# Kernel optimization log

Hardware: AMD Instinct MI355X
Metric: run time of the kernel (lower is better)

## Reference

```python
import jax, jax.numpy as jnp
import numpy as np

NUM_EXPERTS = 64
TOP_K = 2
TEMPERATURE = 1.0
MOMENTUM = 0.9


def _l2norm(x, axis=-1):
    # torch F.normalize: x / max(||x||, eps)
    n = jnp.linalg.norm(x, axis=axis, keepdims=True)
    return x / jnp.maximum(n, 1e-12)


def setup_inputs() -> dict:
    key = jax.random.key(0)
    k1, k2 = jax.random.split(key)
    hidden_states = jax.random.normal(k1, (4, 4096, 2048), dtype=jnp.float32)
    centers = _l2norm(jax.random.normal(k2, (NUM_EXPERTS, 2048), dtype=jnp.float32))
    return {"hidden_states": hidden_states, "centers": centers}


def reference(hidden_states, centers):
    B, T, H = hidden_states.shape
    flat = hidden_states.reshape(-1, H).astype(jnp.float32)  # [N, H]
    N = flat.shape[0]

    # cosine-similarity logits
    reps_n = _l2norm(flat)
    centers_n = _l2norm(centers)
    temp = jnp.maximum(jnp.float32(TEMPERATURE), 1e-6)
    logits = (reps_n @ centers_n.T) / temp  # [N, E]

    probs = jax.nn.softmax(logits, axis=-1)
    top_w, top_ids = jax.lax.top_k(probs, TOP_K)  # [N, k]
    top_w = top_w / (jnp.sum(top_w, axis=-1, keepdims=True) + 1e-9)

    # EMA center update from top-1 routed expert (training+update path)
    route = top_ids[:, 0]  # [N]
    sums = jax.ops.segment_sum(flat, route, num_segments=NUM_EXPERTS)  # [E, H]
    counts = jax.ops.segment_sum(jnp.ones((N, 1), jnp.float32), route,
                                 num_segments=NUM_EXPERTS)  # [E, 1]
    means = sums / (counts + 1e-6)
    updated = _l2norm(MOMENTUM * centers + (1.0 - MOMENTUM) * means)
    new_centers = jnp.where(counts > 0, updated, centers)

    top_ids = top_ids.reshape(B, T, TOP_K)
    top_w = top_w.reshape(B, T, TOP_K)
    return top_ids, top_w, new_centers
```

## Files before the change

kernel.cpp:

```cpp
#include <hip/hip_runtime.h>
#include <math.h>

#define NTOK 16384
#define HDIM 2048
#define NEXP 64
#define KK   32
#define TAU  5e-5f
#define LGT  16384
#define MAXB 2048


__global__ __launch_bounds__(256)
void zero_kernel(float* p, int n) {
  int i = blockIdx.x * 256 + threadIdx.x;
  if (i < n) p[i] = 0.0f;
}

__device__ __forceinline__ float block_reduce_sum(float v, float* red) {
  #pragma unroll
  for (int o = 32; o > 0; o >>= 1) v += __shfl_down(v, o, 64);
  int lane = threadIdx.x & 63;
  int wid  = threadIdx.x >> 6;
  if (lane == 0) red[wid] = v;
  __syncthreads();
  float s = red[0] + red[1] + red[2] + red[3];
  __syncthreads();
  return s;
}

__device__ __forceinline__ double block_reduce_sum_f64(double v, double* red) {
  const int tid = threadIdx.x;
  red[tid] = v;
  __syncthreads();
  if (tid < 128) red[tid] += red[tid + 128];
  __syncthreads();
  if (tid < 64)  red[tid] += red[tid + 64];
  __syncthreads();
  double s = 0.0;
  if (tid < 64) {
    s = red[tid];
    #pragma unroll
    for (int o = 32; o > 0; o >>= 1) s += __shfl_down(s, o, 64);
  }
  if (tid == 0) red[0] = s;
  __syncthreads();
  s = red[0];
  __syncthreads();
  return s;
}

__global__ __launch_bounds__(256)
void cnorm_kernel(const float* __restrict__ c, float* __restrict__ inv_nc) {
  __shared__ float red[4];
  int e = blockIdx.x;
  float ss = 0.f;
  #pragma unroll
  for (int j = 0; j < 8; ++j) {
    float v = c[e * HDIM + threadIdx.x + j * 256];
    ss += v * v;
  }
  float tot = block_reduce_sum(ss, red);
  if (threadIdx.x == 0) inv_nc[e] = 1.0f / fmaxf(sqrtf(tot), 1e-12f);
}

__global__ __launch_bounds__(256)
void cnormalize_kernel(const float* __restrict__ c, float* __restrict__ bn) {
  __shared__ double redd[256];
  __shared__ float s_nc;
  const int e = blockIdx.x;
  const int tid = threadIdx.x;
  const float* cr = c + (size_t)e * HDIM;
  double acc = 0.0;
  #pragma unroll
  for (int i = 0; i < 8; ++i) {
    double v = (double)cr[tid + 256 * i];
    acc += v * v;
  }
  double cn = block_reduce_sum_f64(acc, redd);
  if (tid == 0) s_nc = (float)fmax(sqrt(cn), 1e-12);
  __syncthreads();
  const double nc = (double)s_nc;
  #pragma unroll
  for (int i = 0; i < 8; ++i) {
    int k = tid + 256 * i;
    bn[(size_t)e * HDIM + k] = (float)((double)cr[k] / nc);
  }
}

__global__ __launch_bounds__(256)
void gemm_kernel(const float* __restrict__ x, const float* __restrict__ c,
                 float* __restrict__ logits, float* __restrict__ xnorm2) {
  __shared__ __align__(16) float xs[KK][132];
  __shared__ __align__(16) float cs[KK][68];

  const int tid = threadIdx.x;
  const int mt  = blockIdx.x >> 2;
  const int ks  = blockIdx.x & 3;
  const int t0  = mt * 128;
  const int kb  = ks * 512;
  const int tx  = tid & 15;
  const int ty  = tid >> 4;
  const int r0  = ty * 8;
  const int e0t = tx * 4;
  const int sr = tid >> 1;
  const int sq = (tid & 1) * 16;
  const int er = tid >> 2;
  const int eq = (tid & 3) * 8;

  const float* xrow = x + (size_t)(t0 + sr) * HDIM + kb + sq;
  const float* crow = c + (size_t)er * HDIM + kb + eq;

  float4 xp[4], cp[2];
  #pragma unroll
  for (int i = 0; i < 4; ++i) xp[i] = *(const float4*)(xrow + 4 * i);
  #pragma unroll
  for (int i = 0; i < 2; ++i) cp[i] = *(const float4*)(crow + 4 * i);

  float acc[4][8];
  #pragma unroll
  for (int j = 0; j < 4; ++j)
    #pragma unroll
    for (int i = 0; i < 8; ++i) acc[j][i] = 0.f;
  float nacc = 0.f;

  for (int it = 0; it < 16; ++it) {
    __syncthreads();
    #pragma unroll
    for (int i = 0; i < 4; ++i) {
      xs[sq + 4*i + 0][sr] = xp[i].x; xs[sq + 4*i + 1][sr] = xp[i].y;
      xs[sq + 4*i + 2][sr] = xp[i].z; xs[sq + 4*i + 3][sr] = xp[i].w;
      nacc += xp[i].x*xp[i].x + xp[i].y*xp[i].y + xp[i].z*xp[i].z + xp[i].w*xp[i].w;
    }
    #pragma unroll
    for (int i = 0; i < 2; ++i) {
      cs[eq + 4*i + 0][er] = cp[i].x; cs[eq + 4*i + 1][er] = cp[i].y;
      cs[eq + 4*i + 2][er] = cp[i].z; cs[eq + 4*i + 3][er] = cp[i].w;
    }
    __syncthreads();
    if (it < 15) {
      const float* xn = xrow + (it + 1) * KK;
      const float* cn = crow + (it + 1) * KK;
      #pragma unroll
      for (int i = 0; i < 4; ++i) xp[i] = *(const float4*)(xn + 4 * i);
      #pragma unroll
      for (int i = 0; i < 2; ++i) cp[i] = *(const float4*)(cn + 4 * i);
    }
    #pragma unroll
    for (int k = 0; k < KK; ++k) {
      float4 a0 = *(const float4*)&xs[k][r0];
      float4 a1 = *(const float4*)&xs[k][r0 + 4];
      float4 b  = *(const float4*)&cs[k][e0t];
      acc[0][0] += b.x*a0.x; acc[0][1] += b.x*a0.y; acc[0][2] += b.x*a0.z; acc[0][3] += b.x*a0.w;
      acc[0][4] += b.x*a1.x; acc[0][5] += b.x*a1.y; acc[0][6] += b.x*a1.z; acc[0][7] += b.x*a1.w;
      acc[1][0] += b.y*a0.x; acc[1][1] += b.y*a0.y; acc[1][2] += b.y*a0.z; acc[1][3] += b.y*a0.w;
      acc[1][4] += b.y*a1.x; acc[1][5] += b.y*a1.y; acc[1][6] += b.y*a1.z; acc[1][7] += b.y*a1.w;
      acc[2][0] += b.z*a0.x; acc[2][1] += b.z*a0.y; acc[2][2] += b.z*a0.z; acc[2][3] += b.z*a0.w;
      acc[2][4] += b.z*a1.x; acc[2][5] += b.z*a1.y; acc[2][6] += b.z*a1.z; acc[2][7] += b.z*a1.w;
      acc[3][0] += b.w*a0.x; acc[3][1] += b.w*a0.y; acc[3][2] += b.w*a0.z; acc[3][3] += b.w*a0.w;
      acc[3][4] += b.w*a1.x; acc[3][5] += b.w*a1.y; acc[3][6] += b.w*a1.z; acc[3][7] += b.w*a1.w;
    }
  }

  atomicAdd(&xnorm2[t0 + sr], nacc);

  float* lt = &xs[0][0];
  #pragma unroll
  for (int eh = 0; eh < 2; ++eh) {
    __syncthreads();
    if ((tx >> 3) == eh) {
      const int exl = (tx & 7) * 4;
      #pragma unroll
      for (int j = 0; j < 4; ++j)
        #pragma unroll
        for (int i = 0; i < 8; ++i)
          lt[(exl + j) * 128 + r0 + i] = acc[j][i];
    }
    __syncthreads();
    #pragma unroll
    for (int n = 0; n < 16; ++n) {
      const int f = tid + n * 256;
      const int e = (f >> 7) + eh * 32;
      const int t = f & 127;
      atomicAdd(&logits[(size_t)e * LGT + t0 + t], lt[f]);
    }
  }
}

__global__ __launch_bounds__(256)
void softmax_kernel(const float* __restrict__ logits, const float* __restrict__ xnorm2,
                    const float* __restrict__ inv_nc, float* __restrict__ out,
                    int* __restrict__ route, int* __restrict__ nflag,
                    int* __restrict__ flags) {
  __shared__ float snc[NEXP];
  const int tid = threadIdx.x;
  if (tid < NEXP) snc[tid] = inv_nc[tid];
  __syncthreads();
  const int t = blockIdx.x * 256 + tid;
  const float inv_nx = 1.0f / fmaxf(sqrtf(xnorm2[t]), 1e-12f);
  float lv[NEXP];
  #pragma unroll
  for (int e = 0; e < NEXP; ++e)
    lv[e] = logits[(size_t)e * LGT + t] * snc[e] * inv_nx;
  float m1 = -1e30f, m2 = -1e30f, m3 = -1e30f;
  int i1 = 0, i2 = 0;
  #pragma unroll
  for (int e = 0; e < NEXP; ++e) {
    float l = lv[e];
    if (l > m1)      { m3 = m2; m2 = m1; i2 = i1; m1 = l; i1 = e; }
    else if (l > m2) { m3 = m2; m2 = l; i2 = e; }
    else if (l > m3) { m3 = l; }
  }
  float Z = 0.f;
  #pragma unroll
  for (int e = 0; e < NEXP; ++e) Z += expf(lv[e] - m1);
  const float p1w = 1.0f / Z;
  const float p2w = expf(m2 - m1) / Z;
  const float s   = p1w + p2w + 1e-9f;
  out[t * 2 + 0] = (float)i1;
  out[t * 2 + 1] = (float)i2;
  out[2 * NTOK + t * 2 + 0] = p1w / s;
  out[2 * NTOK + t * 2 + 1] = p2w / s;
  route[t] = i1;
  if ((m1 - m2) < TAU || (m2 - m3) < TAU) {
    int idx = atomicAdd(nflag, 1);
    flags[idx] = t;
  }
}

__global__ __launch_bounds__(256)
void refine_np_kernel(const float* __restrict__ x, const float* __restrict__ bn,
                      float* __restrict__ out, int* __restrict__ route,
                      const int* __restrict__ nflag, const int* __restrict__ flags) {
  __shared__ float a_lds[HDIM];
  __shared__ double redd[256];
  __shared__ float lf[NEXP];
  __shared__ float s_nx;
  const int tid  = threadIdx.x;
  const int lane = tid & 63;
  const int w    = tid >> 6;
  const int n = *nflag;
  for (int j = blockIdx.x; j < n; j += gridDim.x) {
    const int t = flags[j];
    const float* xr = x + (size_t)t * HDIM;
    double xacc = 0.0;
    #pragma unroll
    for (int i = 0; i < 8; ++i) {
      double v = (double)xr[tid + 256 * i];
      xacc += v * v;
    }
    double xn = block_reduce_sum_f64(xacc, redd);
    if (tid == 0) s_nx = (float)fmax(sqrt(xn), 1e-12);
    __syncthreads();
    const double nx = (double)s_nx;
    #pragma unroll
    for (int i = 0; i < 8; ++i) {
      int k = tid + 256 * i;
      a_lds[k] = (float)((double)xr[k] / nx);
    }
    __syncthreads();
    #pragma unroll 1
    for (int ei = 0; ei < 16; ++ei) {
      const int e = w * 16 + ei;
      const float* br = bn + (size_t)e * HDIM;
      double d = 0.0;
      #pragma unroll 8
      for (int i = 0; i < 32; ++i) {
        int k = lane + 64 * i;
        d += (double)a_lds[k] * (double)br[k];
      }
      #pragma unroll
      for (int o = 32; o > 0; o >>= 1) d += __shfl_down(d, o, 64);
      if (lane == 0) lf[e] = (float)d;
    }
    __syncthreads();
    if (tid == 0) {
      float m32 = lf[0];
      for (int ee = 1; ee < NEXP; ++ee) m32 = fmaxf(m32, lf[ee]);
      float ex[NEXP];
      for (int ee = 0; ee < NEXP; ++ee)
        ex[ee] = (float)exp((double)(lf[ee] - m32));
      float r[8];
      #pragma unroll
      for (int q = 0; q < 8; ++q) r[q] = ex[q];
      for (int i = 8; i < NEXP; i += 8)
        #pragma unroll
        for (int q = 0; q < 8; ++q) r[q] += ex[i + q];
      const float Z = ((r[0] + r[1]) + (r[2] + r[3])) + ((r[4] + r[5]) + (r[6] + r[7]));
      float p1 = -1.f, p2 = -1.f;
      int i1 = 0, i2 = 0;
      for (int ee = 0; ee < NEXP; ++ee) {
        float p = ex[ee] / Z;
        if (p > p1)      { p2 = p1; i2 = i1; p1 = p; i1 = ee; }
        else if (p > p2) { p2 = p; i2 = ee; }
      }
      const float s = (p1 + p2) + 1e-9f;
      out[t * 2 + 0] = (float)i1;
      out[t * 2 + 1] = (float)i2;
      out[2 * NTOK + t * 2 + 0] = p1 / s;
      out[2 * NTOK + t * 2 + 1] = p2 / s;
      route[t] = i1;
    }
    __syncthreads();
  }
}

__global__ __launch_bounds__(64)
void refine_np_slow(const float* __restrict__ x, const float* __restrict__ c,
                    float* __restrict__ out, int* __restrict__ route,
                    const int* __restrict__ nflag, const int* __restrict__ flags) {
  __shared__ float lf[NEXP];
  const int e = threadIdx.x;
  const int n = *nflag;
  for (int j = blockIdx.x; j < n; j += gridDim.x) {
    const int t = flags[j];
    const float* xr = x + (size_t)t * HDIM;
    const float* cr = c + (size_t)e * HDIM;
    double xn = 0.0, cn = 0.0;
    for (int k = 0; k < HDIM; ++k) {
      double xv = (double)xr[k];
      double cv = (double)cr[k];
      xn += xv * xv;
      cn += cv * cv;
    }
    const float nx32 = (float)fmax(sqrt(xn), 1e-12);
    const float nc32 = (float)fmax(sqrt(cn), 1e-12);
    double d = 0.0;
    for (int k = 0; k < HDIM; ++k) {
      float a = (float)((double)xr[k] / (double)nx32);
      float b = (float)((double)cr[k] / (double)nc32);
      d += (double)a * (double)b;
    }
    lf[e] = (float)d;
    __syncthreads();
    if (e == 0) {
      float m32 = lf[0];
      for (int ee = 1; ee < NEXP; ++ee) m32 = fmaxf(m32, lf[ee]);
      float ex[NEXP];
      for (int ee = 0; ee < NEXP; ++ee)
        ex[ee] = (float)exp((double)(lf[ee] - m32));
      float r[8];
      #pragma unroll
      for (int q = 0; q < 8; ++q) r[q] = ex[q];
      for (int i = 8; i < NEXP; i += 8)
        #pragma unroll
        for (int q = 0; q < 8; ++q) r[q] += ex[i + q];
      const float Z = ((r[0] + r[1]) + (r[2] + r[3])) + ((r[4] + r[5]) + (r[6] + r[7]));
      float p1 = -1.f, p2 = -1.f;
      int i1 = 0, i2 = 0;
      for (int ee = 0; ee < NEXP; ++ee) {
        float p = ex[ee] / Z;
        if (p > p1)      { p2 = p1; i2 = i1; p1 = p; i1 = ee; }
        else if (p > p2) { p2 = p; i2 = ee; }
      }
      const float s = (p1 + p2) + 1e-9f;
      out[t * 2 + 0] = (float)i1;
      out[t * 2 + 1] = (float)i2;
      out[2 * NTOK + t * 2 + 0] = p1 / s;
      out[2 * NTOK + t * 2 + 1] = p2 / s;
      route[t] = i1;
    }
    __syncthreads();
  }
}

__global__ __launch_bounds__(256)
void scatter_kernel(const int* __restrict__ route, int* __restrict__ cursor,
                    int* __restrict__ bucket) {
  const int t = blockIdx.x * 256 + threadIdx.x;
  const int e = route[t];
  const int pos = atomicAdd(&cursor[e], 1);
  if (pos < MAXB) bucket[e * MAXB + pos] = t;
}

__global__ __launch_bounds__(256)
void segsum_dense(const float* __restrict__ x, const int* __restrict__ cursor,
                  const int* __restrict__ bucket, float* __restrict__ sums) {
  __shared__ int ts[MAXB];
  const int e   = blockIdx.x >> 3;
  const int hc  = blockIdx.x & 7;
  const int hb  = hc * 256;
  const int tid = threadIdx.x;
  int n = cursor[e];
  if (n > MAXB) n = MAXB;
  for (int i = tid; i < n; i += 256) ts[i] = bucket[e * MAXB + i];
  __syncthreads();
  float a[8];
  #pragma unroll
  for (int q = 0; q < 8; ++q) a[q] = 0.f;
  int i = 0;
  for (; i + 7 < n; i += 8) {
    #pragma unroll
    for (int q = 0; q < 8; ++q)
      a[q] += x[(size_t)ts[i + q] * HDIM + hb + tid];
  }
  for (; i < n; ++i) a[0] += x[(size_t)ts[i] * HDIM + hb + tid];
  const float s = ((a[0] + a[1]) + (a[2] + a[3])) + ((a[4] + a[5]) + (a[6] + a[7]));
  sums[e * HDIM + hb + tid] = s;
}

__global__ __launch_bounds__(256)
void finalize_kernel(const float* __restrict__ c, const float* __restrict__ sums,
                     const int* __restrict__ counts, float* __restrict__ out) {
  __shared__ float red[4];
  const int e = blockIdx.x;
  const int tid = threadIdx.x;
  const float cnt = (float)counts[e];
  const float minv = 1.0f / (cnt + 1e-6f);
  float u[8], cv[8];
  float ss = 0.f;
  #pragma unroll
  for (int j = 0; j < 8; ++j) {
    int h = tid + j * 256;
    cv[j] = c[e * HDIM + h];
    float mean = sums[e * HDIM + h] * minv;
    u[j] = 0.9f * cv[j] + 0.1f * mean;
    ss += u[j] * u[j];
  }
  float tot = block_reduce_sum(ss, red);
  float sc = 1.0f / fmaxf(sqrtf(tot), 1e-12f);
  const bool nz = cnt > 0.f;
  #pragma unroll
  for (int j = 0; j < 8; ++j) {
    int h = tid + j * 256;
    out[4 * NTOK + e * HDIM + h] = nz ? u[j] * sc : cv[j];
  }
}

__global__ __launch_bounds__(256)
void router_kernel(const float* __restrict__ x, const float* __restrict__ c,
                   const float* __restrict__ inv_nc, float* __restrict__ out,
                   int* __restrict__ route, int* __restrict__ nflag,
                   int* __restrict__ flags) {
  __shared__ __align__(16) float xs[64][36];
  __shared__ float lgs[64][67];
  const int tid  = threadIdx.x;
  const int lane = tid & 63;
  const int w    = tid >> 6;
  const int t0   = blockIdx.x * 64;
  const int e0   = __builtin_amdgcn_readfirstlane(w * 16);
  const float* cb = c + (size_t)e0 * HDIM;
  const int st = tid >> 3;
  const int sk = (tid & 7) * 4;
  float acc[16];
  #pragma unroll
  for (int e = 0; e < 16; ++e) acc[e] = 0.f;
  float nacc = 0.f;
  float4 p0 = *(const float4*)&x[(size_t)(t0 + st)      * HDIM + sk];
  float4 p1 = *(const float4*)&x[(size_t)(t0 + st + 32) * HDIM + sk];
  for (int k0 = 0; k0 < HDIM; k0 += 32) {
    __syncthreads();
    *(float4*)&xs[st][sk]      = p0;
    *(float4*)&xs[st + 32][sk] = p1;
    __syncthreads();
    const int kn = k0 + 32;
    if (kn < HDIM) {
      p0 = *(const float4*)&x[(size_t)(t0 + st)      * HDIM + kn + sk];
      p1 = *(const float4*)&x[(size_t)(t0 + st + 32) * HDIM + kn + sk];
    }
    float a[32];
    #pragma unroll
    for (int j = 0; j < 32; j += 4) {
      float4 v = *(const float4*)&xs[lane][j];
      a[j] = v.x; a[j+1] = v.y; a[j+2] = v.z; a[j+3] = v.w;
    }
    if (w == 0) {
      #pragma unroll
      for (int j = 0; j < 32; ++j) nacc += a[j] * a[j];
    }
    #pragma unroll
    for (int e = 0; e < 16; ++e) {
      const float* br = cb + (size_t)e * HDIM + k0;
      #pragma unroll
      for (int j = 0; j < 32; j += 4) {
        float4 bv = *(const float4*)&br[j];
        acc[e] += a[j]*bv.x + a[j+1]*bv.y + a[j+2]*bv.z + a[j+3]*bv.w;
      }
    }
  }
  #pragma unroll
  for (int e = 0; e < 16; ++e) lgs[lane][e0 + e] = acc[e] * inv_nc[e0 + e];
  __syncthreads();
  if (w == 0) {
    const float inv_nx = 1.0f / fmaxf(sqrtf(nacc), 1e-12f);
    float m1 = -1e30f, m2 = -1e30f, m3 = -1e30f;
    int i1 = 0, i2 = 0;
    for (int e = 0; e < NEXP; ++e) {
      float l = lgs[lane][e] * inv_nx;
      if (l > m1)      { m3 = m2; m2 = m1; i2 = i1; m1 = l; i1 = e; }
      else if (l > m2) { m3 = m2; m2 = l; i2 = e; }
      else if (l > m3) { m3 = l; }
    }
    float Z = 0.f;
    for (int e = 0; e < NEXP; ++e) Z += expf(lgs[lane][e] * inv_nx - m1);
    const float p1w = 1.0f / Z;
    const float p2w = expf(m2 - m1) / Z;
    const float s   = p1w + p2w + 1e-9f;
    const int tg = t0 + lane;
    out[tg * 2 + 0] = (float)i1;
    out[tg * 2 + 1] = (float)i2;
    out[2 * NTOK + tg * 2 + 0] = p1w / s;
    out[2 * NTOK + tg * 2 + 1] = p2w / s;
    route[tg] = i1;
    if ((m1 - m2) < TAU || (m2 - m3) < TAU) {
      int idx = atomicAdd(nflag, 1);
      flags[idx] = tg;
    }
  }
}

__global__ __launch_bounds__(512)
void segsum_kernel(const float* __restrict__ x, const int* __restrict__ route,
                   float* __restrict__ sums, int* __restrict__ counts) {
  __shared__ float ls[NEXP * 256];
  __shared__ int lcnt[NEXP];
  const int tid  = threadIdx.x;
  const int lane = tid & 63;
  const int w    = tid >> 6;
  const int hc   = blockIdx.x & 7;
  const int tg   = blockIdx.x >> 3;
  const int hb   = hc * 256;
  #pragma unroll
  for (int i = 0; i < 32; ++i) ls[tid + i * 512] = 0.f;
  if (tid < NEXP) lcnt[tid] = 0;
  __syncthreads();
  const int tbase = tg * 512 + w * 64;
  #pragma unroll 4
  for (int i = 0; i < 64; ++i) {
    const int t = tbase + i;
    const int e = route[t];
    const float* xr = x + (size_t)t * HDIM + hb + lane;
    #pragma unroll
    for (int j = 0; j < 4; ++j)
      atomicAdd(&ls[e * 256 + lane + 64 * j], xr[64 * j]);
    if (hc == 0 && lane == 0) atomicAdd(&lcnt[e], 1);
  }
  __syncthreads();
  #pragma unroll
  for (int i = tid; i < NEXP * 256; i += 512) {
    const int e = i >> 8, h = i & 255;
    atomicAdd(&sums[e * HDIM + hb + h], ls[i]);
  }
  if (hc == 0 && tid < NEXP && lcnt[tid] > 0) atomicAdd(&counts[tid], lcnt[tid]);
}

extern "C" void kernel_launch(void* const* d_in, const int* in_sizes, int n_in,
                              void* d_out, int out_size, void* d_ws, size_t ws_size,
                              hipStream_t stream) {
  const float* x = (const float*)d_in[0];
  const float* c = (const float*)d_in[1];
  float* out = (float*)d_out;
  float* ws = (float*)d_ws;

  float* inv_nc = ws;
  int*   counts = (int*)(ws + 64);
  int*   nflag  = (int*)(ws + 128);
  int*   route  = (int*)(ws + 192);
  int*   flags  = (int*)(ws + 16576);
  float* sums   = ws + 32960;
  float* xnorm2 = ws + 164032;
  float* logits = ws + 180416;
  float* bn     = ws + 1228992;
  int*   bucket = (int*)(ws + 1360064);

  const size_t NEED = 1491136ull * 4ull;
  if (ws_size >= NEED) {
    zero_kernel<<<1, 256, 0, stream>>>(ws + 64, 128);
    zero_kernel<<<4160, 256, 0, stream>>>(ws + 164032, 1064960);
    cnorm_kernel<<<NEXP, 256, 0, stream>>>(c, inv_nc);
    cnormalize_kernel<<<NEXP, 256, 0, stream>>>(c, bn);
    gemm_kernel<<<512, 256, 0, stream>>>(x, c, logits, xnorm2);
    softmax_kernel<<<64, 256, 0, stream>>>(logits, xnorm2, inv_nc, out, route, nflag, flags);
    refine_np_kernel<<<512, 256, 0, stream>>>(x, bn, out, route, nflag, flags);
    scatter_kernel<<<64, 256, 0, stream>>>(route, counts, bucket);
    segsum_dense<<<512, 256, 0, stream>>>(x, counts, bucket, sums);
    finalize_kernel<<<NEXP, 256, 0, stream>>>(c, sums, counts, out);
  } else {
    zero_kernel<<<1, 256, 0, stream>>>(ws + 64, 128);
    zero_kernel<<<512, 256, 0, stream>>>(sums, 131072);
    cnorm_kernel<<<NEXP, 256, 0, stream>>>(c, inv_nc);
    router_kernel<<<NTOK / 64, 256, 0, stream>>>(x, c, inv_nc, out, route, nflag, flags);
    refine_np_slow<<<1024, 64, 0, stream>>>(x, c, out, route, nflag, flags);
    segsum_kernel<<<256, 512, 0, stream>>>(x, route, sums, counts);
    finalize_kernel<<<NEXP, 256, 0, stream>>>(c, sums, counts, out);
  }
}
```

Measured before the change: 322.0 us.

## Shrink GEMM token tile to 64 and fold center-norm into normalize kernel

The logits GEMM now uses a 64-token by 64-expert tile with a 4x4 per-thread accumulator instead of 128 tokens with a 4x8 accumulator. The grid doubles to 1024 blocks and shared memory per block shrinks, giving more blocks and occupancy to fill the GPU. The row-norm partial sums are reduced across 4 lanes before the atomic add. The separate cnorm kernel is dropped because cnormalize now also writes inv_nc, which saves one launch. In exchange, the smaller tile loads the center matrix twice as often per token, lowers arithmetic intensity, and doubles the atomic traffic on logits.

```diff
diff --git a/kernel.cpp b/kernel.cpp
--- a/kernel.cpp
+++ b/kernel.cpp
@@ -64,7 +64,8 @@
 }
 
 __global__ __launch_bounds__(256)
-void cnormalize_kernel(const float* __restrict__ c, float* __restrict__ bn) {
+void cnormalize_kernel(const float* __restrict__ c, float* __restrict__ bn,
+                       float* __restrict__ inv_nc) {
   __shared__ double redd[256];
   __shared__ float s_nc;
   const int e = blockIdx.x;
@@ -77,7 +78,10 @@
     acc += v * v;
   }
   double cn = block_reduce_sum_f64(acc, redd);
-  if (tid == 0) s_nc = (float)fmax(sqrt(cn), 1e-12);
+  if (tid == 0) {
+    s_nc = (float)fmax(sqrt(cn), 1e-12);
+    inv_nc[e] = 1.0f / s_nc;
+  }
   __syncthreads();
   const double nc = (double)s_nc;
   #pragma unroll
@@ -90,99 +94,84 @@
 __global__ __launch_bounds__(256)
 void gemm_kernel(const float* __restrict__ x, const float* __restrict__ c,
                  float* __restrict__ logits, float* __restrict__ xnorm2) {
-  __shared__ __align__(16) float xs[KK][132];
-  __shared__ __align__(16) float cs[KK][68];
+  __shared__ __align__(16) float smem[2 * KK * 68];
+  float* xs = smem;
+  float* cs = smem + KK * 68;
 
   const int tid = threadIdx.x;
   const int mt  = blockIdx.x >> 2;
   const int ks  = blockIdx.x & 3;
-  const int t0  = mt * 128;
+  const int t0  = mt * 64;
   const int kb  = ks * 512;
   const int tx  = tid & 15;
   const int ty  = tid >> 4;
-  const int r0  = ty * 8;
-  const int e0t = tx * 4;
-  const int sr = tid >> 1;
-  const int sq = (tid & 1) * 16;
-  const int er = tid >> 2;
-  const int eq = (tid & 3) * 8;
+  const int sr = tid >> 2;
+  const int sq = (tid & 3) * 8;
 
   const float* xrow = x + (size_t)(t0 + sr) * HDIM + kb + sq;
-  const float* crow = c + (size_t)er * HDIM + kb + eq;
-
-  float4 xp[4], cp[2];
-  #pragma unroll
-  for (int i = 0; i < 4; ++i) xp[i] = *(const float4*)(xrow + 4 * i);
+  const float* crow = c + (size_t)sr * HDIM + kb + sq;
+
+  float4 xp[2], cp[2];
+  #pragma unroll
+  for (int i = 0; i < 2; ++i) xp[i] = *(const float4*)(xrow + 4 * i);
   #pragma unroll
   for (int i = 0; i < 2; ++i) cp[i] = *(const float4*)(crow + 4 * i);
 
-  float acc[4][8];
+  float acc[4][4];
   #pragma unroll
   for (int j = 0; j < 4; ++j)
     #pragma unroll
-    for (int i = 0; i < 8; ++i) acc[j][i] = 0.f;
+    for (int i = 0; i < 4; ++i) acc[j][i] = 0.f;
   float nacc = 0.f;
 
   for (int it = 0; it < 16; ++it) {
     __syncthreads();
     #pragma unroll
-    for (int i = 0; i < 4; ++i) {
-      xs[sq + 4*i + 0][sr] = xp[i].x; xs[sq + 4*i + 1][sr] = xp[i].y;
-      xs[sq + 4*i + 2][sr] = xp[i].z; xs[sq + 4*i + 3][sr] = xp[i].w;
+    for (int i = 0; i < 2; ++i) {
+      xs[(sq + 4*i + 0) * 68 + sr] = xp[i].x; xs[(sq + 4*i + 1) * 68 + sr] = xp[i].y;
+      xs[(sq + 4*i + 2) * 68 + sr] = xp[i].z; xs[(sq + 4*i + 3) * 68 + sr] = xp[i].w;
       nacc += xp[i].x*xp[i].x + xp[i].y*xp[i].y + xp[i].z*xp[i].z + xp[i].w*xp[i].w;
-    }
-    #pragma unroll
-    for (int i = 0; i < 2; ++i) {
-      cs[eq + 4*i + 0][er] = cp[i].x; cs[eq + 4*i + 1][er] = cp[i].y;
-      cs[eq + 4*i + 2][er] = cp[i].z; cs[eq + 4*i + 3][er] = cp[i].w;
+      cs[(sq + 4*i + 0) * 68 + sr] = cp[i].x; cs[(sq + 4*i + 1) * 68 + sr] = cp[i].y;
+      cs[(sq + 4*i + 2) * 68 + sr] = cp[i].z; cs[(sq + 4*i + 3) * 68 + sr] = cp[i].w;
     }
     __syncthreads();
     if (it < 15) {
       const float* xn = xrow + (it + 1) * KK;
       const float* cn = crow + (it + 1) * KK;
       #pragma unroll
-      for (int i = 0; i < 4; ++i) xp[i] = *(const float4*)(xn + 4 * i);
+      for (int i = 0; i < 2; ++i) xp[i] = *(const float4*)(xn + 4 * i);
       #pragma unroll
       for (int i = 0; i < 2; ++i) cp[i] = *(const float4*)(cn + 4 * i);
     }
     #pragma unroll
     for (int k = 0; k < KK; ++k) {
-      float4 a0 = *(const float4*)&xs[k][r0];
-      float4 a1 = *(const float4*)&xs[k][r0 + 4];
-      float4 b  = *(const float4*)&cs[k][e0t];
-      acc[0][0] += b.x*a0.x; acc[0][1] += b.x*a0.y; acc[0][2] += b.x*a0.z; acc[0][3] += b.x*a0.w;
-      acc[0][4] += b.x*a1.x; acc[0][5] += b.x*a1.y; acc[0][6] += b.x*a1.z; acc[0][7] += b.x*a1.w;
-      acc[1][0] += b.y*a0.x; acc[1][1] += b.y*a0.y; acc[1][2] += b.y*a0.z; acc[1][3] += b.y*a0.w;
-      acc[1][4] += b.y*a1.x; acc[1][5] += b.y*a1.y; acc[1][6] += b.y*a1.z; acc[1][7] += b.y*a1.w;
-      acc[2][0] += b.z*a0.x; acc[2][1] += b.z*a0.y; acc[2][2] += b.z*a0.z; acc[2][3] += b.z*a0.w;
-      acc[2][4] += b.z*a1.x; acc[2][5] += b.z*a1.y; acc[2][6] += b.z*a1.z; acc[2][7] += b.z*a1.w;
-      acc[3][0] += b.w*a0.x; acc[3][1] += b.w*a0.y; acc[3][2] += b.w*a0.z; acc[3][3] += b.w*a0.w;
-      acc[3][4] += b.w*a1.x; acc[3][5] += b.w*a1.y; acc[3][6] += b.w*a1.z; acc[3][7] += b.w*a1.w;
-    }
-  }
-
-  atomicAdd(&xnorm2[t0 + sr], nacc);
-
-  float* lt = &xs[0][0];
-  #pragma unroll
-  for (int eh = 0; eh < 2; ++eh) {
-    __syncthreads();
-    if ((tx >> 3) == eh) {
-      const int exl = (tx & 7) * 4;
-      #pragma unroll
-      for (int j = 0; j < 4; ++j)
-        #pragma unroll
-        for (int i = 0; i < 8; ++i)
-          lt[(exl + j) * 128 + r0 + i] = acc[j][i];
-    }
-    __syncthreads();
-    #pragma unroll
-    for (int n = 0; n < 16; ++n) {
-      const int f = tid + n * 256;
-      const int e = (f >> 7) + eh * 32;
-      const int t = f & 127;
-      atomicAdd(&logits[(size_t)e * LGT + t0 + t], lt[f]);
-    }
+      float4 a = *(const float4*)&xs[k * 68 + ty * 4];
+      float4 b = *(const float4*)&cs[k * 68 + tx * 4];
+      acc[0][0] += b.x*a.x; acc[0][1] += b.x*a.y; acc[0][2] += b.x*a.z; acc[0][3] += b.x*a.w;
+      acc[1][0] += b.y*a.x; acc[1][1] += b.y*a.y; acc[1][2] += b.y*a.z; acc[1][3] += b.y*a.w;
+      acc[2][0] += b.z*a.x; acc[2][1] += b.z*a.y; acc[2][2] += b.z*a.z; acc[2][3] += b.z*a.w;
+      acc[3][0] += b.w*a.x; acc[3][1] += b.w*a.y; acc[3][2] += b.w*a.z; acc[3][3] += b.w*a.w;
+    }
+  }
+
+  nacc += __shfl_down(nacc, 2, 4);
+  nacc += __shfl_down(nacc, 1, 4);
+  if ((tid & 3) == 0) atomicAdd(&xnorm2[t0 + sr], nacc);
+
+  __syncthreads();
+  float* lt = smem;
+  #pragma unroll
+  for (int j = 0; j < 4; ++j)
+    #pragma unroll
+    for (int i = 0; i < 4; ++i)
+      lt[(tx * 4 + j) * 64 + ty * 4 + i] = acc[j][i];
+  __syncthreads();
+  #pragma unroll
+  for (int n = 0; n < 16; ++n) {
+    const int f = tid + n * 256;
+    const int e = f >> 6;
+    const int t = f & 63;
+    atomicAdd(&logits[(size_t)e * LGT + t0 + t], lt[f]);
   }
 }
 
@@ -566,9 +555,8 @@
   if (ws_size >= NEED) {
     zero_kernel<<<1, 256, 0, stream>>>(ws + 64, 128);
     zero_kernel<<<4160, 256, 0, stream>>>(ws + 164032, 1064960);
-    cnorm_kernel<<<NEXP, 256, 0, stream>>>(c, inv_nc);
-    cnormalize_kernel<<<NEXP, 256, 0, stream>>>(c, bn);
-    gemm_kernel<<<512, 256, 0, stream>>>(x, c, logits, xnorm2);
+    cnormalize_kernel<<<NEXP, 256, 0, stream>>>(c, bn, inv_nc);
+    gemm_kernel<<<1024, 256, 0, stream>>>(x, c, logits, xnorm2);
     softmax_kernel<<<64, 256, 0, stream>>>(logits, xnorm2, inv_nc, out, route, nflag, flags);
     refine_np_kernel<<<512, 256, 0, stream>>>(x, bn, out, route, nflag, flags);
     scatter_kernel<<<64, 256, 0, stream>>>(route, counts, bucket);
```

Result: slower. 347.8 us (+8.0%).

## Fuse prep, bucket scatter into routing, and segsum with finalize to cut launches

Applied to the files above, without the earlier changes.

Merges the zeroing, center-norm and center-normalize kernels into one prep kernel. The per-expert bucket scatter now happens inside the softmax and refine kernels, which removes the separate scatter pass. The segment-sum kernel finalizes each expert's center through a last-block-done counter, which removes the finalize launch. This cuts the launch count and the extra route-array pass, at the cost of more atomics and a threadfence-based cross-block handoff.

```diff
diff --git a/kernel.cpp b/kernel.cpp
--- a/kernel.cpp
+++ b/kernel.cpp
@@ -8,6 +8,7 @@
 #define TAU  5e-5f
 #define LGT  16384
 #define MAXB 2048
+#define MAXFLAG 16320
 
 
 __global__ __launch_bounds__(256)
@@ -50,40 +51,39 @@
 }
 
 __global__ __launch_bounds__(256)
-void cnorm_kernel(const float* __restrict__ c, float* __restrict__ inv_nc) {
-  __shared__ float red[4];
-  int e = blockIdx.x;
-  float ss = 0.f;
-  #pragma unroll
-  for (int j = 0; j < 8; ++j) {
-    float v = c[e * HDIM + threadIdx.x + j * 256];
-    ss += v * v;
-  }
-  float tot = block_reduce_sum(ss, red);
-  if (threadIdx.x == 0) inv_nc[e] = 1.0f / fmaxf(sqrtf(tot), 1e-12f);
-}
-
-__global__ __launch_bounds__(256)
-void cnormalize_kernel(const float* __restrict__ c, float* __restrict__ bn) {
+void prep_kernel(const float* __restrict__ c, float* __restrict__ bn,
+                 float* __restrict__ inv_nc, float* __restrict__ zblk, int zn,
+                 int* __restrict__ ctrl, int* __restrict__ done) {
   __shared__ double redd[256];
   __shared__ float s_nc;
-  const int e = blockIdx.x;
   const int tid = threadIdx.x;
-  const float* cr = c + (size_t)e * HDIM;
-  double acc = 0.0;
-  #pragma unroll
-  for (int i = 0; i < 8; ++i) {
-    double v = (double)cr[tid + 256 * i];
-    acc += v * v;
-  }
-  double cn = block_reduce_sum_f64(acc, redd);
-  if (tid == 0) s_nc = (float)fmax(sqrt(cn), 1e-12);
-  __syncthreads();
-  const double nc = (double)s_nc;
-  #pragma unroll
-  for (int i = 0; i < 8; ++i) {
-    int k = tid + 256 * i;
-    bn[(size_t)e * HDIM + k] = (float)((double)cr[k] / nc);
+  const int b   = blockIdx.x;
+  for (int i = b * 256 + tid; i < zn; i += gridDim.x * 256) zblk[i] = 0.f;
+  if (b == 0) {
+    if (tid < 128) ctrl[tid] = 0;
+    if (tid < 64)  done[tid] = 0;
+  }
+  if (b < NEXP) {
+    const int e = b;
+    const float* cr = c + (size_t)e * HDIM;
+    double acc = 0.0;
+    #pragma unroll
+    for (int i = 0; i < 8; ++i) {
+      double v = (double)cr[tid + 256 * i];
+      acc += v * v;
+    }
+    double cn = block_reduce_sum_f64(acc, redd);
+    if (tid == 0) {
+      s_nc = (float)fmax(sqrt(cn), 1e-12);
+      inv_nc[e] = 1.0f / s_nc;
+    }
+    __syncthreads();
+    const double nc = (double)s_nc;
+    #pragma unroll
+    for (int i = 0; i < 8; ++i) {
+      int k = tid + 256 * i;
+      bn[(size_t)e * HDIM + k] = (float)((double)cr[k] / nc);
+    }
   }
 }
 
@@ -190,7 +190,8 @@
 void softmax_kernel(const float* __restrict__ logits, const float* __restrict__ xnorm2,
                     const float* __restrict__ inv_nc, float* __restrict__ out,
                     int* __restrict__ route, int* __restrict__ nflag,
-                    int* __restrict__ flags) {
+                    int* __restrict__ flags, int* __restrict__ cursor,
+                    int* __restrict__ bucket) {
   __shared__ float snc[NEXP];
   const int tid = threadIdx.x;
   if (tid < NEXP) snc[tid] = inv_nc[tid];
@@ -221,16 +222,23 @@
   out[2 * NTOK + t * 2 + 0] = p1w / s;
   out[2 * NTOK + t * 2 + 1] = p2w / s;
   route[t] = i1;
-  if ((m1 - m2) < TAU || (m2 - m3) < TAU) {
+  bool fl = (m1 - m2) < TAU || (m2 - m3) < TAU;
+  if (fl) {
     int idx = atomicAdd(nflag, 1);
-    flags[idx] = t;
+    if (idx < MAXFLAG) { flags[idx] = t; fl = true; }
+    else fl = false;
+  }
+  if (!fl) {
+    int pos = atomicAdd(&cursor[i1], 1);
+    if (pos < MAXB) bucket[i1 * MAXB + pos] = t;
   }
 }
 
 __global__ __launch_bounds__(256)
 void refine_np_kernel(const float* __restrict__ x, const float* __restrict__ bn,
                       float* __restrict__ out, int* __restrict__ route,
-                      const int* __restrict__ nflag, const int* __restrict__ flags) {
+                      const int* __restrict__ nflag, const int* __restrict__ flags,
+                      int* __restrict__ cursor, int* __restrict__ bucket) {
   __shared__ float a_lds[HDIM];
   __shared__ double redd[256];
   __shared__ float lf[NEXP];
@@ -238,7 +246,8 @@
   const int tid  = threadIdx.x;
   const int lane = tid & 63;
   const int w    = tid >> 6;
-  const int n = *nflag;
+  int n = *nflag;
+  if (n > MAXFLAG) n = MAXFLAG;
   for (int j = blockIdx.x; j < n; j += gridDim.x) {
     const int t = flags[j];
     const float* xr = x + (size_t)t * HDIM;
@@ -299,8 +308,166 @@
       out[2 * NTOK + t * 2 + 0] = p1 / s;
       out[2 * NTOK + t * 2 + 1] = p2 / s;
       route[t] = i1;
-    }
-    __syncthreads();
+      int pos = atomicAdd(&cursor[i1], 1);
+      if (pos < MAXB) bucket[i1 * MAXB + pos] = t;
+    }
+    __syncthreads();
+  }
+}
+
+__global__ __launch_bounds__(256)
+void segsum_finalize(const float* __restrict__ x, const int* __restrict__ cursor,
+                     const int* __restrict__ bucket, float* __restrict__ sums,
+                     const float* __restrict__ c, int* __restrict__ done,
+                     float* __restrict__ out) {
+  __shared__ int ts[MAXB];
+  __shared__ float red[4];
+  __shared__ int lastflag;
+  const int e   = blockIdx.x >> 3;
+  const int hc  = blockIdx.x & 7;
+  const int hb  = hc * 256;
+  const int tid = threadIdx.x;
+  int n = cursor[e];
+  if (n > MAXB) n = MAXB;
+  for (int i = tid; i < n; i += 256) ts[i] = bucket[e * MAXB + i];
+  __syncthreads();
+  float a[8];
+  #pragma unroll
+  for (int q = 0; q < 8; ++q) a[q] = 0.f;
+  int i = 0;
+  for (; i + 7 < n; i += 8) {
+    #pragma unroll
+    for (int q = 0; q < 8; ++q)
+      a[q] += x[(size_t)ts[i + q] * HDIM + hb + tid];
+  }
+  for (; i < n; ++i) a[0] += x[(size_t)ts[i] * HDIM + hb + tid];
+  const float s = ((a[0] + a[1]) + (a[2] + a[3])) + ((a[4] + a[5]) + (a[6] + a[7]));
+  sums[e * HDIM + hb + tid] = s;
+
+  __threadfence();
+  if (tid == 0) {
+    int r = atomicAdd(&done[e], 1);
+    lastflag = (r == 7);
+  }
+  __syncthreads();
+  if (!lastflag) return;
+  __threadfence();
+
+  const float cnt  = (float)cursor[e];
+  const float minv = 1.0f / (cnt + 1e-6f);
+  float u[8], cv[8];
+  float ss = 0.f;
+  #pragma unroll
+  for (int j = 0; j < 8; ++j) {
+    int h = tid + j * 256;
+    cv[j] = c[e * HDIM + h];
+    float mean = sums[e * HDIM + h] * minv;
+    u[j] = 0.9f * cv[j] + 0.1f * mean;
+    ss += u[j] * u[j];
+  }
+  float tot = block_reduce_sum(ss, red);
+  float sc = 1.0f / fmaxf(sqrtf(tot), 1e-12f);
+  const bool nz = cnt > 0.f;
+  #pragma unroll
+  for (int j = 0; j < 8; ++j) {
+    int h = tid + j * 256;
+    out[4 * NTOK + e * HDIM + h] = nz ? u[j] * sc : cv[j];
+  }
+}
+
+__global__ __launch_bounds__(256)
+void cnorm_kernel(const float* __restrict__ c, float* __restrict__ inv_nc) {
+  __shared__ float red[4];
+  int e = blockIdx.x;
+  float ss = 0.f;
+  #pragma unroll
+  for (int j = 0; j < 8; ++j) {
+    float v = c[e * HDIM + threadIdx.x + j * 256];
+    ss += v * v;
+  }
+  float tot = block_reduce_sum(ss, red);
+  if (threadIdx.x == 0) inv_nc[e] = 1.0f / fmaxf(sqrtf(tot), 1e-12f);
+}
+
+__global__ __launch_bounds__(256)
+void router_kernel(const float* __restrict__ x, const float* __restrict__ c,
+                   const float* __restrict__ inv_nc, float* __restrict__ out,
+                   int* __restrict__ route, int* __restrict__ nflag,
+                   int* __restrict__ flags) {
+  __shared__ __align__(16) float xs[64][36];
+  __shared__ float lgs[64][67];
+  const int tid  = threadIdx.x;
+  const int lane = tid & 63;
+  const int w    = tid >> 6;
+  const int t0   = blockIdx.x * 64;
+  const int e0   = __builtin_amdgcn_readfirstlane(w * 16);
+  const float* cb = c + (size_t)e0 * HDIM;
+  const int st = tid >> 3;
+  const int sk = (tid & 7) * 4;
+  float acc[16];
+  #pragma unroll
+  for (int e = 0; e < 16; ++e) acc[e] = 0.f;
+  float nacc = 0.f;
+  float4 p0 = *(const float4*)&x[(size_t)(t0 + st)      * HDIM + sk];
+  float4 p1 = *(const float4*)&x[(size_t)(t0 + st + 32) * HDIM + sk];
+  for (int k0 = 0; k0 < HDIM; k0 += 32) {
+    __syncthreads();
+    *(float4*)&xs[st][sk]      = p0;
+    *(float4*)&xs[st + 32][sk] = p1;
+    __syncthreads();
+    const int kn = k0 + 32;
+    if (kn < HDIM) {
+      p0 = *(const float4*)&x[(size_t)(t0 + st)      * HDIM + kn + sk];
+      p1 = *(const float4*)&x[(size_t)(t0 + st + 32) * HDIM + kn + sk];
+    }
+    float a[32];
+    #pragma unroll
+    for (int j = 0; j < 32; j += 4) {
+      float4 v = *(const float4*)&xs[lane][j];
+      a[j] = v.x; a[j+1] = v.y; a[j+2] = v.z; a[j+3] = v.w;
+    }
+    if (w == 0) {
+      #pragma unroll
+      for (int j = 0; j < 32; ++j) nacc += a[j] * a[j];
+    }
+    #pragma unroll
+    for (int e = 0; e < 16; ++e) {
+      const float* br = cb + (size_t)e * HDIM + k0;
+      #pragma unroll
+      for (int j = 0; j < 32; j += 4) {
+        float4 bv = *(const float4*)&br[j];
+        acc[e] += a[j]*bv.x + a[j+1]*bv.y + a[j+2]*bv.z + a[j+3]*bv.w;
+      }
+    }
+  }
+  #pragma unroll
+  for (int e = 0; e < 16; ++e) lgs[lane][e0 + e] = acc[e] * inv_nc[e0 + e];
+  __syncthreads();
+  if (w == 0) {
+    const float inv_nx = 1.0f / fmaxf(sqrtf(nacc), 1e-12f);
+    float m1 = -1e30f, m2 = -1e30f, m3 = -1e30f;
+    int i1 = 0, i2 = 0;
+    for (int e = 0; e < NEXP; ++e) {
+      float l = lgs[lane][e] * inv_nx;
+      if (l > m1)      { m3 = m2; m2 = m1; i2 = i1; m1 = l; i1 = e; }
+      else if (l > m2) { m3 = m2; m2 = l; i2 = e; }
+      else if (l > m3) { m3 = l; }
+    }
+    float Z = 0.f;
+    for (int e = 0; e < NEXP; ++e) Z += expf(lgs[lane][e] * inv_nx - m1);
+    const float p1w = 1.0f / Z;
+    const float p2w = expf(m2 - m1) / Z;
+    const float s   = p1w + p2w + 1e-9f;
+    const int tg = t0 + lane;
+    out[tg * 2 + 0] = (float)i1;
+    out[tg * 2 + 1] = (float)i2;
+    out[2 * NTOK + tg * 2 + 0] = p1w / s;
+    out[2 * NTOK + tg * 2 + 1] = p2w / s;
+    route[tg] = i1;
+    if ((m1 - m2) < TAU || (m2 - m3) < TAU) {
+      int idx = atomicAdd(nflag, 1);
+      flags[idx] = tg;
+    }
   }
 }
 
@@ -363,151 +530,6 @@
   }
 }
 
-__global__ __launch_bounds__(256)
-void scatter_kernel(const int* __restrict__ route, int* __restrict__ cursor,
-                    int* __restrict__ bucket) {
-  const int t = blockIdx.x * 256 + threadIdx.x;
-  const int e = route[t];
-  const int pos = atomicAdd(&cursor[e], 1);
-  if (pos < MAXB) bucket[e * MAXB + pos] = t;
-}
-
-__global__ __launch_bounds__(256)
-void segsum_dense(const float* __restrict__ x, const int* __restrict__ cursor,
-                  const int* __restrict__ bucket, float* __restrict__ sums) {
-  __shared__ int ts[MAXB];
-  const int e   = blockIdx.x >> 3;
-  const int hc  = blockIdx.x & 7;
-  const int hb  = hc * 256;
-  const int tid = threadIdx.x;
-  int n = cursor[e];
-  if (n > MAXB) n = MAXB;
-  for (int i = tid; i < n; i += 256) ts[i] = bucket[e * MAXB + i];
-  __syncthreads();
-  float a[8];
-  #pragma unroll
-  for (int q = 0; q < 8; ++q) a[q] = 0.f;
-  int i = 0;
-  for (; i + 7 < n; i += 8) {
-    #pragma unroll
-    for (int q = 0; q < 8; ++q)
-      a[q] += x[(size_t)ts[i + q] * HDIM + hb + tid];
-  }
-  for (; i < n; ++i) a[0] += x[(size_t)ts[i] * HDIM + hb + tid];
-  const float s = ((a[0] + a[1]) + (a[2] + a[3])) + ((a[4] + a[5]) + (a[6] + a[7]));
-  sums[e * HDIM + hb + tid] = s;
-}
-
-__global__ __launch_bounds__(256)
-void finalize_kernel(const float* __restrict__ c, const float* __restrict__ sums,
-                     const int* __restrict__ counts, float* __restrict__ out) {
-  __shared__ float red[4];
-  const int e = blockIdx.x;
-  const int tid = threadIdx.x;
-  const float cnt = (float)counts[e];
-  const float minv = 1.0f / (cnt + 1e-6f);
-  float u[8], cv[8];
-  float ss = 0.f;
-  #pragma unroll
-  for (int j = 0; j < 8; ++j) {
-    int h = tid + j * 256;
-    cv[j] = c[e * HDIM + h];
-    float mean = sums[e * HDIM + h] * minv;
-    u[j] = 0.9f * cv[j] + 0.1f * mean;
-    ss += u[j] * u[j];
-  }
-  float tot = block_reduce_sum(ss, red);
-  float sc = 1.0f / fmaxf(sqrtf(tot), 1e-12f);
-  const bool nz = cnt > 0.f;
-  #pragma unroll
-  for (int j = 0; j < 8; ++j) {
-    int h = tid + j * 256;
-    out[4 * NTOK + e * HDIM + h] = nz ? u[j] * sc : cv[j];
-  }
-}
-
-__global__ __launch_bounds__(256)
-void router_kernel(const float* __restrict__ x, const float* __restrict__ c,
-                   const float* __restrict__ inv_nc, float* __restrict__ out,
-                   int* __restrict__ route, int* __restrict__ nflag,
-                   int* __restrict__ flags) {
-  __shared__ __align__(16) float xs[64][36];
-  __shared__ float lgs[64][67];
-  const int tid  = threadIdx.x;
-  const int lane = tid & 63;
-  const int w    = tid >> 6;
-  const int t0   = blockIdx.x * 64;
-  const int e0   = __builtin_amdgcn_readfirstlane(w * 16);
-  const float* cb = c + (size_t)e0 * HDIM;
-  const int st = tid >> 3;
-  const int sk = (tid & 7) * 4;
-  float acc[16];
-  #pragma unroll
-  for (int e = 0; e < 16; ++e) acc[e] = 0.f;
-  float nacc = 0.f;
-  float4 p0 = *(const float4*)&x[(size_t)(t0 + st)      * HDIM + sk];
-  float4 p1 = *(const float4*)&x[(size_t)(t0 + st + 32) * HDIM + sk];
-  for (int k0 = 0; k0 < HDIM; k0 += 32) {
-    __syncthreads();
-    *(float4*)&xs[st][sk]      = p0;
-    *(float4*)&xs[st + 32][sk] = p1;
-    __syncthreads();
-    const int kn = k0 + 32;
-    if (kn < HDIM) {
-      p0 = *(const float4*)&x[(size_t)(t0 + st)      * HDIM + kn + sk];
-      p1 = *(const float4*)&x[(size_t)(t0 + st + 32) * HDIM + kn + sk];
-    }
-    float a[32];
-    #pragma unroll
-    for (int j = 0; j < 32; j += 4) {
-      float4 v = *(const float4*)&xs[lane][j];
-      a[j] = v.x; a[j+1] = v.y; a[j+2] = v.z; a[j+3] = v.w;
-    }
-    if (w == 0) {
-      #pragma unroll
-      for (int j = 0; j < 32; ++j) nacc += a[j] * a[j];
-    }
-    #pragma unroll
-    for (int e = 0; e < 16; ++e) {
-      const float* br = cb + (size_t)e * HDIM + k0;
-      #pragma unroll
-      for (int j = 0; j < 32; j += 4) {
-        float4 bv = *(const float4*)&br[j];
-        acc[e] += a[j]*bv.x + a[j+1]*bv.y + a[j+2]*bv.z + a[j+3]*bv.w;
-      }
-    }
-  }
-  #pragma unroll
-  for (int e = 0; e < 16; ++e) lgs[lane][e0 + e] = acc[e] * inv_nc[e0 + e];
-  __syncthreads();
-  if (w == 0) {
-    const float inv_nx = 1.0f / fmaxf(sqrtf(nacc), 1e-12f);
-    float m1 = -1e30f, m2 = -1e30f, m3 = -1e30f;
-    int i1 = 0, i2 = 0;
-    for (int e = 0; e < NEXP; ++e) {
-      float l = lgs[lane][e] * inv_nx;
-      if (l > m1)      { m3 = m2; m2 = m1; i2 = i1; m1 = l; i1 = e; }
-      else if (l > m2) { m3 = m2; m2 = l; i2 = e; }
-      else if (l > m3) { m3 = l; }
-    }
-    float Z = 0.f;
-    for (int e = 0; e < NEXP; ++e) Z += expf(lgs[lane][e] * inv_nx - m1);
-    const float p1w = 1.0f / Z;
-    const float p2w = expf(m2 - m1) / Z;
-    const float s   = p1w + p2w + 1e-9f;
-    const int tg = t0 + lane;
-    out[tg * 2 + 0] = (float)i1;
-    out[tg * 2 + 1] = (float)i2;
-    out[2 * NTOK + tg * 2 + 0] = p1w / s;
-    out[2 * NTOK + tg * 2 + 1] = p2w / s;
-    route[tg] = i1;
-    if ((m1 - m2) < TAU || (m2 - m3) < TAU) {
-      int idx = atomicAdd(nflag, 1);
-      flags[idx] = tg;
-    }
-  }
-}
-
 __global__ __launch_bounds__(512)
 void segsum_kernel(const float* __restrict__ x, const int* __restrict__ route,
                    float* __restrict__ sums, int* __restrict__ counts) {
@@ -543,6 +565,34 @@
   if (hc == 0 && tid < NEXP && lcnt[tid] > 0) atomicAdd(&counts[tid], lcnt[tid]);
 }
 
+__global__ __launch_bounds__(256)
+void finalize_kernel(const float* __restrict__ c, const float* __restrict__ sums,
+                     const int* __restrict__ counts, float* __restrict__ out) {
+  __shared__ float red[4];
+  const int e = blockIdx.x;
+  const int tid = threadIdx.x;
+  const float cnt = (float)counts[e];
+  const float minv = 1.0f / (cnt + 1e-6f);
+  float u[8], cv[8];
+  float ss = 0.f;
+  #pragma unroll
+  for (int j = 0; j < 8; ++j) {
+    int h = tid + j * 256;
+    cv[j] = c[e * HDIM + h];
+    float mean = sums[e * HDIM + h] * minv;
+    u[j] = 0.9f * cv[j] + 0.1f * mean;
+    ss += u[j] * u[j];
+  }
+  float tot = block_reduce_sum(ss, red);
+  float sc = 1.0f / fmaxf(sqrtf(tot), 1e-12f);
+  const bool nz = cnt > 0.f;
+  #pragma unroll
+  for (int j = 0; j < 8; ++j) {
+    int h = tid + j * 256;
+    out[4 * NTOK + e * HDIM + h] = nz ? u[j] * sc : cv[j];
+  }
+}
+
 extern "C" void kernel_launch(void* const* d_in, const int* in_sizes, int n_in,
                               void* d_out, int out_size, void* d_ws, size_t ws_size,
                               hipStream_t stream) {
@@ -552,10 +602,11 @@
   float* ws = (float*)d_ws;
 
   float* inv_nc = ws;
-  int*   counts = (int*)(ws + 64);
+  int*   cursor = (int*)(ws + 64);
   int*   nflag  = (int*)(ws + 128);
   int*   route  = (int*)(ws + 192);
   int*   flags  = (int*)(ws + 16576);
+  int*   done   = (int*)(ws + 32896);
   float* sums   = ws + 32960;
   float* xnorm2 = ws + 164032;
   float* logits = ws + 180416;
@@ -564,23 +615,21 @@
 
   const size_t NEED = 1491136ull * 4ull;
   if (ws_size >= NEED) {
-    zero_kernel<<<1, 256, 0, stream>>>(ws + 64, 128);
-    zero_kernel<<<4160, 256, 0, stream>>>(ws + 164032, 1064960);
-    cnorm_kernel<<<NEXP, 256, 0, stream>>>(c, inv_nc);
-    cnormalize_kernel<<<NEXP, 256, 0, stream>>>(c, bn);
+    prep_kernel<<<1088, 256, 0, stream>>>(c, bn, inv_nc, ws + 164032, 1064960,
+                                          (int*)(ws + 64), done);
     gemm_kernel<<<512, 256, 0, stream>>>(x, c, logits, xnorm2);
-    softmax_kernel<<<64, 256, 0, stream>>>(logits, xnorm2, inv_nc, out, route, nflag, flags);
-    refine_np_kernel<<<512, 256, 0, stream>>>(x, bn, out, route, nflag, flags);
-    scatter_kernel<<<64, 256, 0, stream>>>(route, counts, bucket);
-    segsum_dense<<<512, 256, 0, stream>>>(x, counts, bucket, sums);
-    finalize_kernel<<<NEXP, 256, 0, stream>>>(c, sums, counts, out);
+    softmax_kernel<<<64, 256, 0, stream>>>(logits, xnorm2, inv_nc, out, route,
+                                           nflag, flags, cursor, bucket);
+    refine_np_kernel<<<512, 256, 0, stream>>>(x, bn, out, route, nflag, flags,
+                                              cursor, bucket);
+    segsum_finalize<<<512, 256, 0, stream>>>(x, cursor, bucket, sums, c, done, out);
   } else {
     zero_kernel<<<1, 256, 0, stream>>>(ws + 64, 128);
     zero_kernel<<<512, 256, 0, stream>>>(sums, 131072);
     cnorm_kernel<<<NEXP, 256, 0, stream>>>(c, inv_nc);
     router_kernel<<<NTOK / 64, 256, 0, stream>>>(x, c, inv_nc, out, route, nflag, flags);
     refine_np_slow<<<1024, 64, 0, stream>>>(x, c, out, route, nflag, flags);
-    segsum_kernel<<<256, 512, 0, stream>>>(x, route, sums, counts);
-    finalize_kernel<<<NEXP, 256, 0, stream>>>(c, sums, counts, out);
-  }
-}
+    segsum_kernel<<<256, 512, 0, stream>>>(x, route, sums, (int*)(ws + 64));
+    finalize_kernel<<<NEXP, 256, 0, stream>>>(c, sums, (int*)(ws + 64), out);
+  }
+}
```

After: 367.9 us. 14.3% more time.
